# Kernel tuning notes

Hardware: AMD Instinct MI355X
Metric: run time of the kernel (lower is better)

Reference implementation:

```python
import jax, jax.numpy as jnp
import numpy as np

B, S, HID = 1, 2048, 3072
NH, NKV, HD = 32, 8, 96
N_REP = NH // NKV
ROPE_THETA = 10000.0


def _rotate_half(x):
    half = x.shape[-1] // 2
    return jnp.concatenate([-x[..., half:], x[..., :half]], axis=-1)


def setup_inputs() -> dict:
    key = jax.random.key(0)
    k1, k2, k3 = jax.random.split(key, 3)
    hidden_states = jax.random.normal(k1, (B, S, HID), dtype=jnp.float32)
    qkv_w = jax.random.normal(k2, (NH * HD + 2 * NKV * HD, HID), dtype=jnp.float32) * 0.02
    o_w = jax.random.normal(k3, (HID, NH * HD), dtype=jnp.float32) * 0.02
    position_ids = jnp.broadcast_to(jnp.arange(S, dtype=jnp.int64)[None, :], (B, S))
    causal = jnp.tril(jnp.ones((S, S), dtype=bool))
    attention_mask = jnp.where(causal, 0.0, jnp.finfo(jnp.float32).min)[None, None].astype(jnp.float32)
    attention_mask = jnp.broadcast_to(attention_mask, (B, 1, S, S))
    return {"hidden_states": hidden_states, "position_ids": position_ids,
            "attention_mask": attention_mask, "qkv_w": qkv_w, "o_w": o_w}


def reference(hidden_states, position_ids, attention_mask, qkv_w, o_w):
    b, s, _ = hidden_states.shape
    qkv = jnp.einsum('bsh,oh->bso', hidden_states, qkv_w)
    q_pos = NH * HD
    q = qkv[..., :q_pos]
    k = qkv[..., q_pos:q_pos + NKV * HD]
    v = qkv[..., q_pos + NKV * HD:]
    # [b, heads, s, hd]
    q = q.reshape(b, s, NH, HD).transpose(0, 2, 1, 3)
    k = k.reshape(b, s, NKV, HD).transpose(0, 2, 1, 3)
    v = v.reshape(b, s, NKV, HD).transpose(0, 2, 1, 3)
    # RoPE
    inv_freq = 1.0 / (ROPE_THETA ** (jnp.arange(0, HD, 2, dtype=jnp.float32) / HD))
    freqs = position_ids.astype(jnp.float32)[:, :, None] * inv_freq[None, None, :]  # [b,s,hd/2]
    emb = jnp.concatenate([freqs, freqs], axis=-1)  # [b,s,hd]
    cos = jnp.cos(emb)[:, None, :, :]
    sin = jnp.sin(emb)[:, None, :, :]
    q = q * cos + _rotate_half(q) * sin
    k = k * cos + _rotate_half(k) * sin
    # GQA repeat_kv (repeat_interleave on head dim)
    k = jnp.repeat(k, N_REP, axis=1)
    v = jnp.repeat(v, N_REP, axis=1)
    scores = jnp.einsum('bhqd,bhkd->bhqk', q, k) / jnp.sqrt(jnp.float32(HD))
    scores = scores + attention_mask
    w = jax.nn.softmax(scores.astype(jnp.float32), axis=-1).astype(v.dtype)
    attn = jnp.einsum('bhqk,bhkd->bhqd', w, v)
    attn = attn.transpose(0, 2, 1, 3).reshape(b, s, NH * HD)
    out = jnp.einsum('bsf,of->bso', attn, o_w)
    return out
```

## Files before the change

kernel.cpp:

```cpp
#include <hip/hip_runtime.h>

#define S_LEN 2048
#define HID_DIM 3072
#define NH 32
#define NKV 8
#define HD 96
#define QKV_OUT 4608

typedef __attribute__((ext_vector_type(8))) short short8;
typedef __attribute__((ext_vector_type(4))) float floatx4;

__device__ __forceinline__ unsigned short f2b(float f) {
    unsigned int u = __float_as_uint(f);
    u = (u + 0x7FFFu + ((u >> 16) & 1u)) >> 16;
    return (unsigned short)u;
}
__device__ __forceinline__ float b2f(unsigned short h) {
    return __uint_as_float(((unsigned int)h) << 16);
}
__device__ __forceinline__ void async_ld16(const void* g, void* l) {
    __builtin_amdgcn_global_load_lds((const __attribute__((address_space(1))) void*)g,
                                     (__attribute__((address_space(3))) void*)l, 16, 0, 0);
}
__device__ __forceinline__ float fast_exp2(float x) {
#if __has_builtin(__builtin_amdgcn_exp2f)
    return __builtin_amdgcn_exp2f(x);
#else
    return exp2f(x);
#endif
}
__device__ __forceinline__ void store_out(float* C, size_t i, float v) { C[i] = v; }
__device__ __forceinline__ void store_out(unsigned short* C, size_t i, float v) { C[i] = f2b(v); }


__global__ void cvt3_tiled(const float* __restrict__ a, int nab,
                           const float* __restrict__ b, int nbb,
                           const float* __restrict__ c, int ncb,
                           unsigned short* __restrict__ oa,
                           unsigned short* __restrict__ ob,
                           unsigned short* __restrict__ oc) {
    int wid = blockIdx.x * 4 + (threadIdx.x >> 6);
    const int l = threadIdx.x & 63;
    const float* src;
    unsigned short* dst;
    int j = wid;
    if (j < nab) { src = a; dst = oa; }
    else {
        j -= nab;
        if (j < nbb) { src = b; dst = ob; }
        else {
            j -= nbb;
            if (j >= ncb) return;
            src = c; dst = oc;
        }
    }
    const int KB = HID_DIM >> 5;
    int rt = j / KB, kc = j - rt * KB;
    int i = l & 15, q = l >> 4;
    const float* p = src + ((size_t)rt * 16 + i) * HID_DIM + kc * 32 + q * 8;
    float4 v0 = *(const float4*)p;
    float4 v1 = *(const float4*)(p + 4);
    short8 o;
    o[0] = (short)f2b(v0.x); o[1] = (short)f2b(v0.y);
    o[2] = (short)f2b(v0.z); o[3] = (short)f2b(v0.w);
    o[4] = (short)f2b(v1.x); o[5] = (short)f2b(v1.y);
    o[6] = (short)f2b(v1.z); o[7] = (short)f2b(v1.w);
    *(short8*)(dst + (size_t)j * 512 + l * 8) = o;
}

template <typename OUT>
__global__ void gemm_bt(const unsigned short* __restrict__ A,
                        const unsigned short* __restrict__ B,
                        OUT* __restrict__ C, int M, int N, int K) {
    __shared__ unsigned short As[8 * 512];
    __shared__ unsigned short Bs[24 * 512];
    const int KB = K >> 5;
    const int t = threadIdx.x;
    const int w = t >> 6;
    const int l = t & 63;
    const int lane15 = l & 15;
    const int quad = l >> 4;
    const int rowt = blockIdx.y * 4;
    const int colt = blockIdx.x * 12;

    const floatx4 vzero = {0.f, 0.f, 0.f, 0.f};
    floatx4 acc[4][4];
#pragma unroll
    for (int i = 0; i < 4; ++i)
#pragma unroll
        for (int j = 0; j < 4; ++j) acc[i][j] = vzero;

    for (int kc0 = 0; kc0 < KB; kc0 += 2) {
        __syncthreads();
#pragma unroll
        for (int j = 0; j < 11; ++j) {
            int s = w + j * 3;
            if (s < 32) {
                if (s < 8) {
                    int x = s >> 1, kkb = s & 1;
                    size_t ablk = (size_t)(rowt + x) * KB + kc0 + kkb;
                    async_ld16(A + ablk * 512 + l * 8, As + s * 512 + l * 8);
                } else {
                    int s2 = s - 8;
                    int x = s2 >> 1, kkb = s2 & 1;
                    size_t bblk = (size_t)(colt + x) * KB + kc0 + kkb;
                    async_ld16(B + bblk * 512 + l * 8, Bs + s2 * 512 + l * 8);
                }
            }
        }
        __syncthreads();
#pragma unroll
        for (int kkb = 0; kkb < 2; ++kkb) {
            short8 af[4], bfr[4];
#pragma unroll
            for (int mi = 0; mi < 4; ++mi)
                af[mi] = *(const short8*)(As + (mi * 2 + kkb) * 512 + l * 8);
#pragma unroll
            for (int ni = 0; ni < 4; ++ni)
                bfr[ni] = *(const short8*)(Bs + ((w * 4 + ni) * 2 + kkb) * 512 + l * 8);
#pragma unroll
            for (int mi = 0; mi < 4; ++mi)
#pragma unroll
                for (int ni = 0; ni < 4; ++ni)
                    acc[mi][ni] = __builtin_amdgcn_mfma_f32_16x16x32_bf16(af[mi], bfr[ni], acc[mi][ni], 0, 0, 0);
        }
    }
#pragma unroll
    for (int mi = 0; mi < 4; ++mi)
#pragma unroll
        for (int ni = 0; ni < 4; ++ni)
#pragma unroll
            for (int r = 0; r < 4; ++r) {
                int m = rowt * 16 + mi * 16 + quad * 4 + r;
                int n = (colt + w * 4 + ni) * 16 + lane15;
                store_out(C, (size_t)m * N + n, acc[mi][ni][r]);
            }
}

__global__ void rope_split(const unsigned short* __restrict__ qkv,
                           unsigned short* __restrict__ Qd,
                           unsigned short* __restrict__ Kd,
                           unsigned short* __restrict__ Vd) {
    const int s = blockIdx.x;
    const int t = threadIdx.x;
    const unsigned short* row = qkv + (size_t)s * QKV_OUT;
    const float L2T_48 = 0.2768273412406135f;
    const float SCALE2 = 0.14724444f;

    for (int i = t; i < NH * 48; i += 256) {
        int h = i / 48, d = i - (i / 48) * 48;
        float f = (float)s * exp2f(-(float)d * L2T_48);
        float sn, cs;
        sincosf(f, &sn, &cs);
        float q1 = b2f(row[h * 96 + d]);
        float q2 = b2f(row[h * 96 + d + 48]);
        size_t base = ((size_t)h * S_LEN + s) * HD;
        Qd[base + d] = f2b((q1 * cs - q2 * sn) * SCALE2);
        Qd[base + d + 48] = f2b((q2 * cs + q1 * sn) * SCALE2);
    }
    for (int i = t; i < NKV * 48; i += 256) {
        int h = i / 48, d = i - (i / 48) * 48;
        float f = (float)s * exp2f(-(float)d * L2T_48);
        float sn, cs;
        sincosf(f, &sn, &cs);
        float k1 = b2f(row[3072 + h * 96 + d]);
        float k2 = b2f(row[3072 + h * 96 + d + 48]);
        size_t base = ((size_t)h * S_LEN + s) * HD;
        Kd[base + d] = f2b(k1 * cs - k2 * sn);
        Kd[base + d + 48] = f2b(k2 * cs + k1 * sn);
    }
    for (int i = t; i < NKV * HD; i += 256) {
        int h = i / 96, d = i - (i / 96) * 96;
        Vd[((size_t)h * S_LEN + s) * HD + d] = row[3840 + i];
    }
}

__global__ void transpose_v(const unsigned short* __restrict__ V,
                            unsigned short* __restrict__ Vt) {
    __shared__ unsigned short T[96][72];
    const int kvh = blockIdx.x >> 5;
    const int s0 = (blockIdx.x & 31) * 64;
    const int t = threadIdx.x;
#pragma unroll
    for (int it = 0; it < 3; ++it) {
        int c = it * 256 + t;
        int r = c / 12, c8 = c - r * 12;
        short8 v = *(const short8*)(V + ((size_t)kvh * S_LEN + s0 + r) * HD + c8 * 8);
#pragma unroll
        for (int j = 0; j < 8; ++j) T[c8 * 8 + j][r] = (unsigned short)v[j];
    }
    __syncthreads();
#pragma unroll
    for (int it = 0; it < 3; ++it) {
        int c = it * 256 + t;
        int d = c >> 3, c8 = c & 7;
        short8 v;
#pragma unroll
        for (int j = 0; j < 8; ++j) v[j] = (short)T[d][c8 * 8 + j];
        *(short8*)(Vt + ((size_t)kvh * HD + d) * S_LEN + s0 + c8 * 8) = v;
    }
}

#define ATTN_M0 8.0f
__global__ __launch_bounds__(256) void attn_fwd(const unsigned short* __restrict__ Q,
                                                const unsigned short* __restrict__ K,
                                                const unsigned short* __restrict__ Vt,
                                                unsigned short* __restrict__ O) {
    __shared__ unsigned short Qs[4 * 3 * 512];
    __shared__ unsigned short Ks[12 * 512];
    __shared__ unsigned short Vs[12 * 512];
    __shared__ unsigned short Ps[4][16 * 72];
    const int h = blockIdx.x;
    const int qt = (int)gridDim.y - 1 - blockIdx.y;
    const int kvh = h >> 2;
    const int q0 = qt * 64;
    const int t = threadIdx.x, w = t >> 6, l = t & 63;
    const int lane15 = l & 15, quad = l >> 4;
    unsigned short* Pw = Ps[w];

    const unsigned short* Qg = Q + ((size_t)h * S_LEN + q0) * HD;
#pragma unroll
    for (int kkb = 0; kkb < 3; ++kkb)
        async_ld16(Qg + (w * 16 + lane15) * HD + kkb * 32 + quad * 8,
                   Qs + (w * 3 + kkb) * 512 + l * 8);

    int koff[3], voff0[3];
    long vofS[3];
#pragma unroll
    for (int j = 0; j < 3; ++j) {
        int c = w * 3 + j;
        int ct = c & 3, kkb = c >> 2;
        koff[j] = (ct * 16 + lane15) * HD + kkb * 32 + quad * 8;
        int nt = c % 6, kb2 = c / 6;
        vofS[j] = (long)(nt * 16 + lane15) * S_LEN + kb2 * 32 + quad * 8;
        voff0[j] = c * 512 + l * 8;
    }

    const floatx4 vzero = {0.f, 0.f, 0.f, 0.f};
    floatx4 accO[6];
#pragma unroll
    for (int nt = 0; nt < 6; ++nt) accO[nt] = vzero;
    float lsum[4] = {0.f, 0.f, 0.f, 0.f};

    const unsigned short* Kg = K + (size_t)kvh * S_LEN * HD;
    const unsigned short* Vg = Vt + (size_t)kvh * HD * S_LEN;
    const int qrow0 = q0 + w * 16 + quad * 4;

    for (int kt = 0; kt <= qt; ++kt) {
        const int k0 = kt * 64;
        __syncthreads();
#pragma unroll
        for (int j = 0; j < 3; ++j) {
            int c = w * 3 + j;
            async_ld16(Kg + (size_t)k0 * HD + koff[j], Ks + c * 512 + l * 8);
            async_ld16(Vg + k0 + vofS[j], Vs + voff0[j]);
        }
        __syncthreads();

        floatx4 accS[4];
#pragma unroll
        for (int ct = 0; ct < 4; ++ct) accS[ct] = vzero;
#pragma unroll
        for (int kkb = 0; kkb < 3; ++kkb) {
            short8 aq = *(const short8*)(Qs + (w * 3 + kkb) * 512 + l * 8);
#pragma unroll
            for (int ct = 0; ct < 4; ++ct) {
                short8 bk = *(const short8*)(Ks + (kkb * 4 + ct) * 512 + l * 8);
                accS[ct] = __builtin_amdgcn_mfma_f32_16x16x32_bf16(aq, bk, accS[ct], 0, 0, 0);
            }
        }

        if (kt < qt) {
#pragma unroll
            for (int ct = 0; ct < 4; ++ct)
#pragma unroll
                for (int r = 0; r < 4; ++r) {
                    float p = fast_exp2(accS[ct][r] - ATTN_M0);
                    lsum[r] += p;
                    Pw[(quad * 4 + r) * 72 + ct * 16 + lane15] = f2b(p);
                }
        } else {
#pragma unroll
            for (int ct = 0; ct < 4; ++ct) {
                int kcol = k0 + ct * 16 + lane15;
#pragma unroll
                for (int r = 0; r < 4; ++r) {
                    float s = (kcol <= qrow0 + r) ? accS[ct][r] - ATTN_M0 : -1.0e30f;
                    float p = fast_exp2(s);
                    lsum[r] += p;
                    Pw[(quad * 4 + r) * 72 + ct * 16 + lane15] = f2b(p);
                }
            }
        }

#pragma unroll
        for (int kb2 = 0; kb2 < 2; ++kb2) {
            short8 ap = *(const short8*)(Pw + lane15 * 72 + kb2 * 32 + quad * 8);
#pragma unroll
            for (int nt = 0; nt < 6; ++nt) {
                short8 bv = *(const short8*)(Vs + (kb2 * 6 + nt) * 512 + l * 8);
                accO[nt] = __builtin_amdgcn_mfma_f32_16x16x32_bf16(ap, bv, accO[nt], 0, 0, 0);
            }
        }
    }

    for (int off = 1; off < 16; off <<= 1)
#pragma unroll
        for (int r = 0; r < 4; ++r) lsum[r] += __shfl_xor(lsum[r], off, 64);
    float inv[4];
#pragma unroll
    for (int r = 0; r < 4; ++r) inv[r] = 1.f / lsum[r];
    const int srow0 = q0 + w * 16 + quad * 4;
#pragma unroll
    for (int nt = 0; nt < 6; ++nt) {
        int n = h * HD + nt * 16 + lane15;
        size_t base = ((size_t)(srow0 >> 4) * (HID_DIM >> 5) + (n >> 5)) * 512
                      + ((n & 31) >> 3) * 128 + (n & 7);
#pragma unroll
        for (int r = 0; r < 4; ++r) {
            int m15 = (srow0 + r) & 15;
            O[base + m15 * 8] = f2b(accO[nt][r] * inv[r]);
        }
    }
}

extern "C" void kernel_launch(void* const* d_in, const int* in_sizes, int n_in,
                              void* d_out, int out_size, void* d_ws, size_t ws_size,
                              hipStream_t stream) {
    const float* hidden = (const float*)d_in[0];
    const float* qkv_w = (const float*)d_in[3];
    const float* o_w = (const float*)d_in[4];
    float* out = (float*)d_out;

    unsigned short* Xb = (unsigned short*)d_ws;
    unsigned short* Wq = Xb + (size_t)S_LEN * HID_DIM;
    unsigned short* Wo = Wq + (size_t)QKV_OUT * HID_DIM;
    unsigned short* QKVb = Wo + (size_t)HID_DIM * HID_DIM;
    unsigned short* Qb = QKVb + (size_t)S_LEN * QKV_OUT;
    unsigned short* Kb = Qb + (size_t)NH * S_LEN * HD;
    unsigned short* Vb = Kb + (size_t)NKV * S_LEN * HD;
    unsigned short* Ab = Vb + (size_t)NKV * S_LEN * HD;
    unsigned short* Vtb = QKVb;

    int nab = S_LEN * HID_DIM / 512, nbb = QKV_OUT * HID_DIM / 512, ncb = HID_DIM * HID_DIM / 512;
    int nblk = nab + nbb + ncb;
    cvt3_tiled<<<nblk / 4, 256, 0, stream>>>(hidden, nab, qkv_w, nbb, o_w, ncb, Xb, Wq, Wo);

    gemm_bt<unsigned short><<<dim3(QKV_OUT / 192, S_LEN / 64), 192, 0, stream>>>(
        Xb, Wq, QKVb, S_LEN, QKV_OUT, HID_DIM);
    rope_split<<<S_LEN, 256, 0, stream>>>(QKVb, Qb, Kb, Vb);
    transpose_v<<<NKV * (S_LEN / 64), 256, 0, stream>>>(Vb, Vtb);
    attn_fwd<<<dim3(NH, S_LEN / 64), 256, 0, stream>>>(Qb, Kb, Vtb, Ab);
    gemm_bt<float><<<dim3(HID_DIM / 192, S_LEN / 64), 192, 0, stream>>>(
        Ab, Wo, out, S_LEN, HID_DIM, HID_DIM);
}
```

Before: 350.3 us.

## Double-buffer GEMM LDS tiles with async prefetch and retile to 128x96 blocks

Replaces the single-buffered GEMM with a double-buffered pipeline that issues the async global-to-LDS loads for the next K-chunk before computing the current one, waiting with vmcnt instead of a full barrier-bracketed load phase. The block tile changes from 64x192 with 3 waves to 128x96 with 4 waves arranged 2x2, each wave computing 4x3 MFMA tiles. s_setprio is raised during the MFMA phase. This aims to hide global load latency behind compute, at the cost of doubled LDS use and a changed tile shape that may alter reuse and occupancy.

Result: faster. 333.6 us (-4.8%).

```diff
diff --git a/kernel.cpp b/kernel.cpp
--- a/kernel.cpp
+++ b/kernel.cpp
@@ -69,70 +69,92 @@
 }
 
 template <typename OUT>
-__global__ void gemm_bt(const unsigned short* __restrict__ A,
-                        const unsigned short* __restrict__ B,
-                        OUT* __restrict__ C, int M, int N, int K) {
-    __shared__ unsigned short As[8 * 512];
-    __shared__ unsigned short Bs[24 * 512];
+__global__ __launch_bounds__(256, 2) void gemm_pipe(const unsigned short* __restrict__ A,
+                                                    const unsigned short* __restrict__ B,
+                                                    OUT* __restrict__ C, int M, int N, int K) {
+    __shared__ unsigned short lds[2][28 * 512];
     const int KB = K >> 5;
-    const int t = threadIdx.x;
-    const int w = t >> 6;
-    const int l = t & 63;
-    const int lane15 = l & 15;
-    const int quad = l >> 4;
-    const int rowt = blockIdx.y * 4;
-    const int colt = blockIdx.x * 12;
+    const int NT = K >> 6;
+    const int t = threadIdx.x, w = t >> 6, l = t & 63;
+    const int lane15 = l & 15, quad = l >> 4;
+    const int wm = (w >> 1) * 4;
+    const int wn = (w & 1) * 3;
+    const int rowt0 = blockIdx.y * 8;
+    const int colt0 = blockIdx.x * 6;
 
     const floatx4 vzero = {0.f, 0.f, 0.f, 0.f};
-    floatx4 acc[4][4];
+    floatx4 acc[4][3];
 #pragma unroll
     for (int i = 0; i < 4; ++i)
 #pragma unroll
-        for (int j = 0; j < 4; ++j) acc[i][j] = vzero;
-
-    for (int kc0 = 0; kc0 < KB; kc0 += 2) {
-        __syncthreads();
-#pragma unroll
-        for (int j = 0; j < 11; ++j) {
-            int s = w + j * 3;
-            if (s < 32) {
-                if (s < 8) {
-                    int x = s >> 1, kkb = s & 1;
-                    size_t ablk = (size_t)(rowt + x) * KB + kc0 + kkb;
-                    async_ld16(A + ablk * 512 + l * 8, As + s * 512 + l * 8);
-                } else {
-                    int s2 = s - 8;
-                    int x = s2 >> 1, kkb = s2 & 1;
-                    size_t bblk = (size_t)(colt + x) * KB + kc0 + kkb;
-                    async_ld16(B + bblk * 512 + l * 8, Bs + s2 * 512 + l * 8);
-                }
-            }
-        }
-        __syncthreads();
+        for (int j = 0; j < 3; ++j) acc[i][j] = vzero;
+
+    const unsigned short* gsrc[7];
+    int ldst[7];
+#pragma unroll
+    for (int j = 0; j < 7; ++j) {
+        int s = w * 7 + j;
+        if (s < 16) {
+            gsrc[j] = A + ((size_t)(rowt0 + (s >> 1)) * KB + (s & 1)) * 512 + l * 8;
+        } else {
+            int s2 = s - 16;
+            gsrc[j] = B + ((size_t)(colt0 + (s2 >> 1)) * KB + (s2 & 1)) * 512 + l * 8;
+        }
+        ldst[j] = s * 512 + l * 8;
+    }
+
+#define STAGE(T)                                                             \
+    {                                                                        \
+        unsigned short* base_ = &lds[(T) & 1][0];                            \
+        size_t koff_ = (size_t)(T) * 1024;                                   \
+        _Pragma("unroll")                                                    \
+        for (int j = 0; j < 7; ++j)                                          \
+            async_ld16(gsrc[j] + koff_, base_ + ldst[j]);                    \
+    }
+
+    STAGE(0);
+    for (int T = 0; T < NT; ++T) {
+        if (T + 1 < NT) {
+            STAGE(T + 1);
+            asm volatile("s_waitcnt vmcnt(7)" ::: "memory");
+        } else {
+            asm volatile("s_waitcnt vmcnt(0)" ::: "memory");
+        }
+        __builtin_amdgcn_s_barrier();
+        asm volatile("" ::: "memory");
+        __builtin_amdgcn_s_setprio(1);
+
+        const unsigned short* buf = &lds[T & 1][0];
 #pragma unroll
         for (int kkb = 0; kkb < 2; ++kkb) {
-            short8 af[4], bfr[4];
+            short8 af[4], bf[3];
 #pragma unroll
             for (int mi = 0; mi < 4; ++mi)
-                af[mi] = *(const short8*)(As + (mi * 2 + kkb) * 512 + l * 8);
-#pragma unroll
-            for (int ni = 0; ni < 4; ++ni)
-                bfr[ni] = *(const short8*)(Bs + ((w * 4 + ni) * 2 + kkb) * 512 + l * 8);
+                af[mi] = *(const short8*)(buf + ((wm + mi) * 2 + kkb) * 512 + l * 8);
+#pragma unroll
+            for (int ni = 0; ni < 3; ++ni)
+                bf[ni] = *(const short8*)(buf + (16 + (wn + ni) * 2 + kkb) * 512 + l * 8);
 #pragma unroll
             for (int mi = 0; mi < 4; ++mi)
 #pragma unroll
-                for (int ni = 0; ni < 4; ++ni)
-                    acc[mi][ni] = __builtin_amdgcn_mfma_f32_16x16x32_bf16(af[mi], bfr[ni], acc[mi][ni], 0, 0, 0);
-        }
-    }
+                for (int ni = 0; ni < 3; ++ni)
+                    acc[mi][ni] = __builtin_amdgcn_mfma_f32_16x16x32_bf16(af[mi], bf[ni], acc[mi][ni], 0, 0, 0);
+        }
+
+        __builtin_amdgcn_s_setprio(0);
+        asm volatile("" ::: "memory");
+        __builtin_amdgcn_s_barrier();
+    }
+#undef STAGE
+
 #pragma unroll
     for (int mi = 0; mi < 4; ++mi)
 #pragma unroll
-        for (int ni = 0; ni < 4; ++ni)
+        for (int ni = 0; ni < 3; ++ni)
 #pragma unroll
             for (int r = 0; r < 4; ++r) {
-                int m = rowt * 16 + mi * 16 + quad * 4 + r;
-                int n = (colt + w * 4 + ni) * 16 + lane15;
+                int m = rowt0 * 16 + (w >> 1) * 64 + mi * 16 + quad * 4 + r;
+                int n = colt0 * 16 + (w & 1) * 48 + ni * 16 + lane15;
                 store_out(C, (size_t)m * N + n, acc[mi][ni][r]);
             }
 }
@@ -346,11 +368,11 @@
     int nblk = nab + nbb + ncb;
     cvt3_tiled<<<nblk / 4, 256, 0, stream>>>(hidden, nab, qkv_w, nbb, o_w, ncb, Xb, Wq, Wo);
 
-    gemm_bt<unsigned short><<<dim3(QKV_OUT / 192, S_LEN / 64), 192, 0, stream>>>(
+    gemm_pipe<unsigned short><<<dim3(QKV_OUT / 96, S_LEN / 128), 256, 0, stream>>>(
         Xb, Wq, QKVb, S_LEN, QKV_OUT, HID_DIM);
     rope_split<<<S_LEN, 256, 0, stream>>>(QKVb, Qb, Kb, Vb);
     transpose_v<<<NKV * (S_LEN / 64), 256, 0, stream>>>(Vb, Vtb);
     attn_fwd<<<dim3(NH, S_LEN / 64), 256, 0, stream>>>(Qb, Kb, Vtb, Ab);
-    gemm_bt<float><<<dim3(HID_DIM / 192, S_LEN / 64), 192, 0, stream>>>(
+    gemm_pipe<float><<<dim3(HID_DIM / 96, S_LEN / 128), 256, 0, stream>>>(
         Ab, Wo, out, S_LEN, HID_DIM, HID_DIM);
 }
```
